# Performance work log

Hardware: AMD Instinct MI355X
Metric: run time of the kernel (lower is better)

Reference implementation:

```python
import jax, jax.numpy as jnp
import numpy as np

# --- model dims (from init_kwargs: d_model=2048, num_heads=16, d_conv=4, expand_v=2) ---
D_MODEL = 2048
N_HEADS = 16
D_HEAD = D_MODEL // N_HEADS          # 128
EXPAND_V = 2
KEY_DIM = N_HEADS * D_HEAD           # 2048
VALUE_DIM = KEY_DIM * EXPAND_V       # 4096
HEAD_V = D_HEAD * EXPAND_V           # 256
D_CONV = 4
CONV_CH = 2 * KEY_DIM + VALUE_DIM    # 8192 (q,k,v channels)
TOTAL_PROJ = 2 * KEY_DIM + 2 * VALUE_DIM + 2 * N_HEADS  # 12320
SPLITS = np.cumsum([KEY_DIM, KEY_DIM, VALUE_DIM, VALUE_DIM, N_HEADS]).tolist()


def setup_inputs() -> dict:
    key = jax.random.key(0)
    k0, k1, k2, k3 = jax.random.split(key, 4)
    B, L = 2, 2048
    return {
        "hidden_states": jax.random.normal(k0, (B, L, D_MODEL), jnp.float32),
        "W_qkvgba": jax.random.normal(k1, (D_MODEL, TOTAL_PROJ), jnp.float32) * 0.02,
        "W_conv": jax.random.normal(k2, (CONV_CH, D_CONV), jnp.float32) * 0.1,
        "A_log": jax.random.normal(k3, (N_HEADS,), jnp.float32) * 0.1,
        "dt_bias": jnp.zeros((N_HEADS,), jnp.float32),
    }


def _l2norm(x, eps=1e-6):
    return x * jax.lax.rsqrt(jnp.sum(x * x, axis=-1, keepdims=True) + eps)


def reference(hidden_states, W_qkvgba, W_conv, A_log, dt_bias):
    B, L, _ = hidden_states.shape
    # fused qkv / gate / beta / A projection
    proj = hidden_states @ W_qkvgba                      # [B, L, 12320]
    q, k, v, gate, b, A = jnp.split(proj, SPLITS, axis=-1)

    # depthwise causal short conv over q,k,v channels, then SiLU
    qkv = jnp.concatenate([q, k, v], axis=-1)            # [B, L, CONV_CH]
    x = qkv.transpose(0, 2, 1)                           # [B, C, L]
    kern = W_conv[:, None, :]                            # [C, 1, D_CONV]
    y = jax.lax.conv_general_dilated(
        x, kern, window_strides=(1,), padding=[(D_CONV - 1, 0)],
        feature_group_count=CONV_CH)
    y = jax.nn.silu(y).transpose(0, 2, 1)                # [B, L, C]
    q, k, v = jnp.split(y, [KEY_DIM, 2 * KEY_DIM], axis=-1)

    q = q.reshape(B, L, N_HEADS, D_HEAD)
    k = k.reshape(B, L, N_HEADS, D_HEAD)
    v = v.reshape(B, L, N_HEADS, HEAD_V)

    # L2 norm of q,k (use_qk_l2norm_in_kernel=True)
    q = _l2norm(q)
    k = _l2norm(k)
    scale = D_HEAD ** -0.5

    beta = jax.nn.sigmoid(b)                             # [B, L, H]
    g = -jnp.exp(A_log) * jax.nn.softplus(A + dt_bias)   # [B, L, H] (log decay <= 0)

    # gated delta-rule recurrence over time (scan); state S: [B, H, dk, dv]
    qT = q.transpose(1, 0, 2, 3)
    kT = k.transpose(1, 0, 2, 3)
    vT = v.transpose(1, 0, 2, 3)
    gT = g.transpose(1, 0, 2)
    bT = beta.transpose(1, 0, 2)

    def step(S, inp):
        qt, kt, vt, gt, bt = inp
        S = S * jnp.exp(gt)[..., None, None]
        kv = jnp.einsum('bhk,bhkv->bhv', kt, S)          # current memory readout at k
        delta = (vt - kv) * bt[..., None]                # delta-rule error, gated by beta
        S = S + jnp.einsum('bhk,bhv->bhkv', kt, delta)
        ot = jnp.einsum('bhk,bhkv->bhv', qt * scale, S)
        return S, ot

    S0 = jnp.zeros((B, N_HEADS, D_HEAD, HEAD_V), jnp.float32)
    _, oT = jax.lax.scan(step, S0, (qT, kT, vT, gT, bT))
    o = oT.transpose(1, 0, 2, 3)                         # [B, L, H, HEAD_V]

    # output gating: o * silu(gate)
    gate = gate.reshape(B, L, N_HEADS, HEAD_V)
    return o * jax.nn.silu(gate)
```

## Files before the change

### kernel.cpp

```cpp
#include <hip/hip_runtime.h>
#include <hip/hip_bf16.h>
#include <hip/hip_fp16.h>
#include <math.h>

#define L_SEQ 2048
#define DM    2048
#define NH    16
#define DH    128
#define HVD   256
#define NPROJ 12320
#define QKVW  8192
#define GW    4128

#define NTILE_N 97
#define KSTEPS  64

typedef _Float16 v8h __attribute__((ext_vector_type(8)));
typedef float f32x4 __attribute__((ext_vector_type(4)));

__device__ __forceinline__ void gload_lds16(const void* g, void* l) {
  __builtin_amdgcn_global_load_lds((const __attribute__((address_space(1))) void*)g,
                                   (__attribute__((address_space(3))) void*)l, 16, 0, 0);
}

__device__ __forceinline__ void splitw(float x, unsigned short& h, unsigned short& l) {
  _Float16 hh = (_Float16)x;
  _Float16 ll = (_Float16)(x - (float)hh);
  h = *(unsigned short*)&hh;
  l = *(unsigned short*)&ll;
}
__device__ __forceinline__ float h2f(unsigned short u) {
  return (float)(*(_Float16*)&u);
}

#define MFMA3(acc, ah, al, bh_, bl_)                                          \
  acc = __builtin_amdgcn_mfma_f32_16x16x32_f16(ah, bh_, acc, 0, 0, 0);        \
  acc = __builtin_amdgcn_mfma_f32_16x16x32_f16(ah, bl_, acc, 0, 0, 0);        \
  acc = __builtin_amdgcn_mfma_f32_16x16x32_f16(al, bh_, acc, 0, 0, 0);

__global__ __launch_bounds__(256) void pack_A_k(const float* __restrict__ H, _Float16* __restrict__ Ap) {
  const int mtile = blockIdx.x >> 6, kstep = blockIdx.x & 63;
  const size_t base = (size_t)blockIdx.x * 2 * 4096;
#pragma unroll
  for (int it = 0; it < 2; ++it) {
    int s = threadIdx.x + it * 256;
    int g = s >> 7, r = s & 127;
    const float* src = H + ((size_t)(mtile * 128 + r)) * 2048 + kstep * 32 + g * 8;
    float4 x0 = *(const float4*)src;
    float4 x1 = *(const float4*)(src + 4);
    float xs[8] = {x0.x, x0.y, x0.z, x0.w, x1.x, x1.y, x1.z, x1.w};
    v8h hi, lo;
#pragma unroll
    for (int j = 0; j < 8; ++j) {
      float v = xs[j] * 16.f;
      _Float16 h = (_Float16)v;
      hi[j] = h;
      lo[j] = (_Float16)(v - (float)h);
    }
    *(v8h*)(Ap + base + g * 1024 + r * 8) = hi;
    *(v8h*)(Ap + base + 4096 + g * 1024 + r * 8) = lo;
  }
}

__global__ __launch_bounds__(256) void pack_B_k(const float* __restrict__ W, _Float16* __restrict__ Bp) {
  const int ntile = blockIdx.x >> 6, kstep = blockIdx.x & 63;
  const size_t base = (size_t)blockIdx.x * 2 * 4096;
#pragma unroll
  for (int it = 0; it < 2; ++it) {
    int s = threadIdx.x + it * 256;
    int g = s >> 7, col = s & 127;
    int n = ntile * 128 + col;
    v8h hi, lo;
#pragma unroll
    for (int j = 0; j < 8; ++j) {
      int k = kstep * 32 + g * 8 + j;
      float v = (n < NPROJ) ? W[(size_t)k * NPROJ + n] * 1024.f : 0.f;
      _Float16 h = (_Float16)v;
      hi[j] = h;
      lo[j] = (_Float16)(v - (float)h);
    }
    *(v8h*)(Bp + base + g * 1024 + col * 8) = hi;
    *(v8h*)(Bp + base + 4096 + g * 1024 + col * 8) = lo;
  }
}

__global__ __launch_bounds__(512, 2) void gemm256_k(const _Float16* __restrict__ Ap,
                                                    const _Float16* __restrict__ Bp,
                                                    float* __restrict__ Cq,
                                                    float* __restrict__ Cg) {
  __shared__ _Float16 lds[2][32768];
  const int tid = threadIdx.x;
  const int supM = blockIdx.x & 15;
  const int supN = blockIdx.x >> 4;
  const int w = tid >> 6, lane = tid & 63;
  const int wm = w >> 2, wn = w & 3;
  const int lr = lane & 15, g16 = lane >> 4;

  f32x4 acc[8][4];
#pragma unroll
  for (int i = 0; i < 8; ++i)
#pragma unroll
    for (int j = 0; j < 4; ++j) acc[i][j] = (f32x4){0.f, 0.f, 0.f, 0.f};

  const size_t Ab0 = (size_t)(2 * supM) * KSTEPS * 8192;
  const size_t Ab1 = Ab0 + (size_t)KSTEPS * 8192;
  const size_t Bb0 = (size_t)(2 * supN) * KSTEPS * 8192;
  const size_t Bb1 = Bb0 + (size_t)KSTEPS * 8192;
  const int so = tid * 8;

#define STG(KS, BUF)                                                           \
  {                                                                            \
    const size_t ko = (size_t)(KS) * 8192;                                     \
    gload_lds16(Ap + Ab0 + ko + so,        &lds[BUF][so]);                     \
    gload_lds16(Ap + Ab0 + ko + so + 4096, &lds[BUF][so + 4096]);              \
    gload_lds16(Ap + Ab1 + ko + so,        &lds[BUF][8192 + so]);              \
    gload_lds16(Ap + Ab1 + ko + so + 4096, &lds[BUF][8192 + so + 4096]);       \
    gload_lds16(Bp + Bb0 + ko + so,        &lds[BUF][16384 + so]);             \
    gload_lds16(Bp + Bb0 + ko + so + 4096, &lds[BUF][16384 + so + 4096]);      \
    gload_lds16(Bp + Bb1 + ko + so,        &lds[BUF][24576 + so]);             \
    gload_lds16(Bp + Bb1 + ko + so + 4096, &lds[BUF][24576 + so + 4096]);      \
  }

  STG(0, 0);
  asm volatile("s_waitcnt vmcnt(0)" ::: "memory");
  __builtin_amdgcn_sched_barrier(0);
  __builtin_amdgcn_s_barrier();
  __builtin_amdgcn_sched_barrier(0);

  const int aoffB = wm * 8192 + lr * 8 + g16 * 1024;
  const int boffB = 16384 + (wn >> 1) * 8192 + ((wn & 1) * 64 + lr) * 8 + g16 * 1024;

  for (int kstep = 0; kstep < KSTEPS; ++kstep) {
    const int p = kstep & 1;
    if (kstep + 1 < KSTEPS) STG(kstep + 1, p ^ 1);

    v8h ah[8], al[8];
#pragma unroll
    for (int mb = 0; mb < 8; ++mb) {
      ah[mb] = *(const v8h*)&lds[p][aoffB + mb * 128];
      al[mb] = *(const v8h*)&lds[p][aoffB + mb * 128 + 4096];
    }
#pragma unroll
    for (int nt = 0; nt < 4; ++nt) {
      v8h bh = *(const v8h*)&lds[p][boffB + nt * 128];
      v8h bl = *(const v8h*)&lds[p][boffB + nt * 128 + 4096];
#pragma unroll
      for (int mb = 0; mb < 8; ++mb) {
        MFMA3(acc[mb][nt], ah[mb], al[mb], bh, bl);
      }
    }
    asm volatile("s_waitcnt vmcnt(0)" ::: "memory");
    __builtin_amdgcn_sched_barrier(0);
    __builtin_amdgcn_s_barrier();
    __builtin_amdgcn_sched_barrier(0);
  }
#undef STG

  const float sc = 1.f / 16384.f;
#pragma unroll
  for (int mb = 0; mb < 8; ++mb) {
#pragma unroll
    for (int nt = 0; nt < 4; ++nt) {
      int col = supN * 256 + wn * 64 + nt * 16 + lr;
#pragma unroll
      for (int r = 0; r < 4; ++r) {
        int row = supM * 256 + wm * 128 + mb * 16 + g16 * 4 + r;
        float v = acc[mb][nt][r] * sc;
        if (col < QKVW) Cq[(size_t)row * QKVW + col] = v;
        else            Cg[(size_t)row * GW + (col - QKVW)] = v;
      }
    }
  }
}

__global__ __launch_bounds__(256) void gemm_mfma_k(const _Float16* __restrict__ Ap,
                                                   const _Float16* __restrict__ Bp,
                                                   float* __restrict__ Cq,
                                                   float* __restrict__ Cg,
                                                   int ntile_base) {
  __shared__ _Float16 lds[2][16384];
  const int tid = threadIdx.x;
  const int mtile = blockIdx.x & 31;
  const int ntile = ntile_base + (blockIdx.x >> 5);
  const int wid = tid >> 6, lane = tid & 63;
  const int wm = wid >> 1, wn = wid & 1;
  const int lrow = lane & 15, g = lane >> 4;

  f32x4 acc[4][4];
#pragma unroll
  for (int i = 0; i < 4; ++i)
#pragma unroll
    for (int j = 0; j < 4; ++j) acc[i][j] = (f32x4){0.f, 0.f, 0.f, 0.f};

  const int aoff = (wm * 64 + lrow) * 8 + g * 1024;
  const int boff = (wn * 64 + lrow) * 8 + g * 1024;

  const _Float16* Asrc = Ap + ((size_t)(mtile * KSTEPS) * 2) * 4096 + tid * 8;
  const _Float16* Bsrc = Bp + ((size_t)(ntile * KSTEPS) * 2) * 4096 + tid * 8;

#define STAGE(KS, BUF)                                                         \
  {                                                                            \
    const _Float16* An_ = Asrc + (size_t)(KS) * 8192;                          \
    const _Float16* Bn_ = Bsrc + (size_t)(KS) * 8192;                          \
    _Pragma("unroll")                                                          \
    for (int r = 0; r < 4; ++r) {                                              \
      gload_lds16(An_ + r * 2048, &lds[BUF][r * 2048 + tid * 8]);              \
      gload_lds16(Bn_ + r * 2048, &lds[BUF][8192 + r * 2048 + tid * 8]);       \
    }                                                                          \
  }

  STAGE(0, 0);
  STAGE(1, 1);

  for (int kstep = 0; kstep < KSTEPS; ++kstep) {
    const int p = kstep & 1;
    if (kstep + 1 < KSTEPS) {
      asm volatile("s_waitcnt vmcnt(8)" ::: "memory");
    } else {
      asm volatile("s_waitcnt vmcnt(0)" ::: "memory");
    }
    __builtin_amdgcn_sched_barrier(0);
    __builtin_amdgcn_s_barrier();
    __builtin_amdgcn_sched_barrier(0);

    v8h ah[4], al[4], bh[4], bl[4];
#pragma unroll
    for (int f = 0; f < 4; ++f) {
      ah[f] = *(const v8h*)&lds[p][aoff + f * 128];
      al[f] = *(const v8h*)&lds[p][4096 + aoff + f * 128];
      bh[f] = *(const v8h*)&lds[p][8192 + boff + f * 128];
      bl[f] = *(const v8h*)&lds[p][12288 + boff + f * 128];
    }
#pragma unroll
    for (int fm = 0; fm < 4; ++fm)
#pragma unroll
      for (int fn = 0; fn < 4; ++fn) {
        acc[fm][fn] = __builtin_amdgcn_mfma_f32_16x16x32_f16(ah[fm], bh[fn], acc[fm][fn], 0, 0, 0);
        acc[fm][fn] = __builtin_amdgcn_mfma_f32_16x16x32_f16(ah[fm], bl[fn], acc[fm][fn], 0, 0, 0);
        acc[fm][fn] = __builtin_amdgcn_mfma_f32_16x16x32_f16(al[fm], bh[fn], acc[fm][fn], 0, 0, 0);
      }
    __builtin_amdgcn_sched_barrier(0);
    __builtin_amdgcn_s_barrier();
    __builtin_amdgcn_sched_barrier(0);
    if (kstep + 2 < KSTEPS) STAGE(kstep + 2, p);
  }
#undef STAGE

  const float sc = 1.f / 16384.f;
#pragma unroll
  for (int fm = 0; fm < 4; ++fm) {
    int row = mtile * 128 + wm * 64 + fm * 16 + g * 4;
#pragma unroll
    for (int fn = 0; fn < 4; ++fn) {
      int col = ntile * 128 + wn * 64 + fn * 16 + lrow;
      if (col < QKVW) {
#pragma unroll
        for (int r = 0; r < 4; ++r)
          Cq[(size_t)(row + r) * QKVW + col] = acc[fm][fn][r] * sc;
      } else if (col < NPROJ) {
        int lcol = col - QKVW;
#pragma unroll
        for (int r = 0; r < 4; ++r)
          Cg[(size_t)(row + r) * GW + lcol] = acc[fm][fn][r] * sc;
      }
    }
  }
}

__global__ __launch_bounds__(64) void conv_qk_k(
    const float* __restrict__ projQKV, const float* __restrict__ Wc,
    _Float16* __restrict__ qh, _Float16* __restrict__ ql,
    _Float16* __restrict__ kh, _Float16* __restrict__ kl)
{
  const int b = blockIdx.z, hg = blockIdx.y, tc = blockIdx.x;
  const int lane = threadIdx.x;
  const int ch = hg * 128 + lane * 2;
  float4 Wa = *(const float4*)(Wc + (size_t)ch * 4);
  float4 Wb = *(const float4*)(Wc + (size_t)ch * 4 + 4);
  const int t0 = tc * 64;
  const float* P = projQKV + (size_t)b * L_SEQ * QKVW + ch;
  float2 w0 = make_float2(0.f, 0.f), w1 = w0, w2 = w0;
  if (t0 >= 3) w0 = *(const float2*)(P + (size_t)(t0 - 3) * QKVW);
  if (t0 >= 2) w1 = *(const float2*)(P + (size_t)(t0 - 2) * QKVW);
  if (t0 >= 1) w2 = *(const float2*)(P + (size_t)(t0 - 1) * QKVW);
  const bool isq = hg < 16;
  const int h = isq ? hg : hg - 16;
  _Float16* dh = (isq ? qh : kh) + (((size_t)b * NH + h) * L_SEQ) * 128;
  _Float16* dl = (isq ? ql : kl) + (((size_t)b * NH + h) * L_SEQ) * 128;
  const float sc = (isq ? 0.08838834764831845f : 1.f) * 1024.f;
  for (int t = t0; t < t0 + 64; ++t) {
    float2 x = *(const float2*)(P + (size_t)t * QKVW);
    float y0 = w0.x * Wa.x + w1.x * Wa.y + w2.x * Wa.z + x.x * Wa.w;
    float y1 = w0.y * Wb.x + w1.y * Wb.y + w2.y * Wb.z + x.y * Wb.w;
    w0 = w1; w1 = w2; w2 = x;
    y0 = y0 / (1.f + expf(-y0));
    y1 = y1 / (1.f + expf(-y1));
    float ss = y0 * y0 + y1 * y1;
#pragma unroll
    for (int off = 1; off < 64; off <<= 1) ss += __shfl_xor(ss, off);
    float nrm = sc / sqrtf(ss + 1e-6f);
    unsigned short h0, l0, h1, l1;
    splitw(y0 * nrm, h0, l0);
    splitw(y1 * nrm, h1, l1);
    int idx = t * 128 + ((lane * 2) ^ ((t & 7) << 3));
    *(unsigned int*)&dh[idx] = (unsigned int)h0 | ((unsigned int)h1 << 16);
    *(unsigned int*)&dl[idx] = (unsigned int)l0 | ((unsigned int)l1 << 16);
  }
}

__global__ __launch_bounds__(256) void conv_v_k(
    const float* __restrict__ projQKV, const float* __restrict__ Wc,
    float* __restrict__ vn)
{
  const int b = blockIdx.z, cg = blockIdx.y, tc = blockIdx.x;
  const int vc = (cg * 256 + threadIdx.x) * 4;
  const int ch = 4096 + vc;
  float4 Wv0 = *(const float4*)(Wc + (size_t)ch * 4);
  float4 Wv1 = *(const float4*)(Wc + (size_t)ch * 4 + 4);
  float4 Wv2 = *(const float4*)(Wc + (size_t)ch * 4 + 8);
  float4 Wv3 = *(const float4*)(Wc + (size_t)ch * 4 + 12);
  const int t0 = tc * 64;
  const float* P = projQKV + (size_t)b * L_SEQ * QKVW + ch;
  float4 w0 = make_float4(0.f, 0.f, 0.f, 0.f), w1 = w0, w2 = w0;
  if (t0 >= 3) w0 = *(const float4*)(P + (size_t)(t0 - 3) * QKVW);
  if (t0 >= 2) w1 = *(const float4*)(P + (size_t)(t0 - 2) * QKVW);
  if (t0 >= 1) w2 = *(const float4*)(P + (size_t)(t0 - 1) * QKVW);
  const int h = vc >> 8, vcol = vc & 255;
  float* dst = vn + (((size_t)b * NH + h) * L_SEQ) * HVD + vcol;
  for (int t = t0; t < t0 + 64; ++t) {
    float4 x = *(const float4*)(P + (size_t)t * QKVW);
    float4 y;
    y.x = w0.x * Wv0.x + w1.x * Wv0.y + w2.x * Wv0.z + x.x * Wv0.w;
    y.y = w0.y * Wv1.x + w1.y * Wv1.y + w2.y * Wv1.z + x.y * Wv1.w;
    y.z = w0.z * Wv2.x + w1.z * Wv2.y + w2.z * Wv2.z + x.z * Wv2.w;
    y.w = w0.w * Wv3.x + w1.w * Wv3.y + w2.w * Wv3.z + x.w * Wv3.w;
    w0 = w1; w1 = w2; w2 = x;
    y.x = y.x / (1.f + expf(-y.x));
    y.y = y.y / (1.f + expf(-y.y));
    y.z = y.z / (1.f + expf(-y.z));
    y.w = y.w / (1.f + expf(-y.w));
    *(float4*)(dst + (size_t)t * HVD) = y;
  }
}

__global__ __launch_bounds__(256) void beta_g_k(
    const float* __restrict__ projGate, const float* __restrict__ A_log,
    const float* __restrict__ dt_bias, float* __restrict__ beta, float* __restrict__ g_out)
{
  int idx = blockIdx.x * 256 + threadIdx.x;
  if (idx >= 2 * NH * L_SEQ) return;
  int t = idx & (L_SEQ - 1);
  int h = (idx >> 11) & (NH - 1);
  int b = idx >> 15;
  size_t row = (size_t)(b * L_SEQ + t) * GW;
  float bv = projGate[row + 4096 + h];
  float av = projGate[row + 4112 + h];
  float be = 1.f / (1.f + expf(-bv));
  float xx = av + dt_bias[h];
  float sp = (xx > 20.f) ? xx : log1pf(expf(xx));
  float g = -expf(A_log[h]) * sp;
  beta[idx] = be;
  g_out[idx] = g;
}

__global__ __launch_bounds__(256) void p1_k(
    const _Float16* __restrict__ kh_g, const _Float16* __restrict__ kl_g,
    const _Float16* __restrict__ qh_g, const _Float16* __restrict__ ql_g,
    const float* __restrict__ g_arr, const float* __restrict__ beta_arr,
    _Float16* __restrict__ Tg_h, _Float16* __restrict__ Tg_l,
    _Float16* __restrict__ Hg_h, _Float16* __restrict__ Hg_l,
    _Float16* __restrict__ KTg_h, _Float16* __restrict__ KTg_l,
    float* __restrict__ coefG)
{
  __shared__ _Float16 Kh[8192], Kl[8192];
  __shared__ _Float16 QS[16384];
  __shared__ float lc[64], be[64], kw[64];
  _Float16* Qh = QS;
  _Float16* Ql = QS + 8192;
  float* Am = (float*)QS;
  float* Tm = Am + 4096;
  const int cid = blockIdx.x, bh = cid >> 5, ch = cid & 31, t0 = ch * 64;
  const int tid = threadIdx.x, w = tid >> 6, lane = tid & 63, lr = lane & 15, g16 = lane >> 4;

  const size_t gb = ((size_t)bh * 2048 + t0) * 128;
#pragma unroll
  for (int l = 0; l < 4; ++l) {
    int i = (tid + l * 256) * 8;
    gload_lds16(kh_g + gb + i, &Kh[i]);
    gload_lds16(kl_g + gb + i, &Kl[i]);
    gload_lds16(qh_g + gb + i, &Qh[i]);
    gload_lds16(ql_g + gb + i, &Ql[i]);
  }
  if (tid < 64) {
    float x = g_arr[(size_t)bh * 2048 + t0 + tid];
#pragma unroll
    for (int off = 1; off < 64; off <<= 1) { float y = __shfl_up(x, off); if (tid >= off) x += y; }
    lc[tid] = x;
    float x63 = __shfl(x, 63);
    float b_ = beta_arr[(size_t)bh * 2048 + t0 + tid];
    be[tid] = b_;
    kw[tid] = expf(x63 - x);
    float ca = expf(x);
    coefG[(size_t)cid * 192 + tid] = ca;
    coefG[(size_t)cid * 192 + 64 + tid] = b_;
    coefG[(size_t)cid * 192 + 128 + tid] = b_ * ca;
  }
  __syncthreads();
  const float ds20 = 1.f / 1048576.f;
  const int arow = w * 16 + lr, swa = (arow & 7) << 3;
  f32x4 gacc[4];
  for (int nt = 0; nt < 4; ++nt) {
    f32x4 acc = (f32x4){0.f, 0.f, 0.f, 0.f};
    int nrow = nt * 16 + lr, swn = (nrow & 7) << 3;
#pragma unroll
    for (int ks = 0; ks < 4; ++ks) {
      int c = ks * 32 + g16 * 8;
      v8h ah = *(const v8h*)&Kh[arow * 128 + (c ^ swa)];
      v8h al = *(const v8h*)&Kl[arow * 128 + (c ^ swa)];
      v8h bhh = *(const v8h*)&Kh[nrow * 128 + (c ^ swn)];
      v8h bll = *(const v8h*)&Kl[nrow * 128 + (c ^ swn)];
      MFMA3(acc, ah, al, bhh, bll);
    }
    gacc[nt] = acc;
  }
  for (int nt = 0; nt < 4; ++nt) {
    f32x4 acc = (f32x4){0.f, 0.f, 0.f, 0.f};
    int nrow = nt * 16 + lr, swn = (nrow & 7) << 3;
#pragma unroll
    for (int ks = 0; ks < 4; ++ks) {
      int c = ks * 32 + g16 * 8;
      v8h ah = *(const v8h*)&Qh[arow * 128 + (c ^ swa)];
      v8h al = *(const v8h*)&Ql[arow * 128 + (c ^ swa)];
      v8h bhh = *(const v8h*)&Kh[nrow * 128 + (c ^ swn)];
      v8h bll = *(const v8h*)&Kl[nrow * 128 + (c ^ swn)];
      MFMA3(acc, ah, al, bhh, bll);
    }
    int s_ = nt * 16 + lr;
#pragma unroll
    for (int r = 0; r < 4; ++r) {
      int t = w * 16 + g16 * 4 + r;
      float hv = (s_ <= t) ? acc[r] * ds20 * expf(lc[t] - lc[s_]) : 0.f;
      unsigned short hh, ll; splitw(hv * 16384.f, hh, ll);
      size_t go = (size_t)cid * 4096 + t * 64 + (s_ ^ ((t & 7) << 3));
      *(unsigned short*)&Hg_h[go] = hh;
      *(unsigned short*)&Hg_l[go] = ll;
    }
  }
  __syncthreads();
  for (int nt = 0; nt < 4; ++nt) {
    int s_ = nt * 16 + lr;
#pragma unroll
    for (int r = 0; r < 4; ++r) {
      int t = w * 16 + g16 * 4 + r;
      float av = (s_ < t) ? gacc[nt][r] * ds20 * be[t] * expf(lc[t] - lc[s_]) : 0.f;
      Am[t * 64 + s_] = av;
    }
  }
#pragma unroll
  for (int l = 0; l < 16; ++l) { int s2 = tid + l * 256; Tm[s2] = ((s2 >> 6) == (s2 & 63)) ? 1.f : 0.f; }
  for (int s = tid; s < 8192; s += 256) {
    int feat = s >> 6, t = s & 63;
    int ki = t * 128 + (feat ^ ((t & 7) << 3));
    float kvv = ((float)Kh[ki] + (float)Kl[ki]) * kw[t];
    unsigned short hh, ll; splitw(kvv, hh, ll);
    size_t go = (size_t)cid * 8192 + feat * 64 + (t ^ ((feat & 7) << 3));
    *(unsigned short*)&KTg_h[go] = hh;
    *(unsigned short*)&KTg_l[go] = ll;
  }
  __syncthreads();
  if (w == 0) {
    int j = lane;
    for (int t = 1; t < 64; ++t) {
      float sum = 0.f;
      for (int s = 0; s < t; ++s) sum = fmaf(Am[t * 64 + s], Tm[s * 64 + j], sum);
      Tm[t * 64 + j] = ((j == t) ? 1.f : 0.f) - sum;
    }
  }
  __syncthreads();
#pragma unroll
  for (int l = 0; l < 16; ++l) {
    int s2 = tid + l * 256;
    int t = s2 >> 6, sc_ = s2 & 63;
    unsigned short hh, ll; splitw(Tm[s2] * 256.f, hh, ll);
    size_t go = (size_t)cid * 4096 + t * 64 + (sc_ ^ ((t & 7) << 3));
    *(unsigned short*)&Tg_h[go] = hh;
    *(unsigned short*)&Tg_l[go] = ll;
  }
}

__global__ __launch_bounds__(256) void p2_k(
    const _Float16* __restrict__ qh_g, const _Float16* __restrict__ ql_g,
    const _Float16* __restrict__ kh_g, const _Float16* __restrict__ kl_g,
    const float* __restrict__ vn, const float* __restrict__ projGate,
    const _Float16* __restrict__ Tg_h, const _Float16* __restrict__ Tg_l,
    const _Float16* __restrict__ Hg_h, const _Float16* __restrict__ Hg_l,
    const _Float16* __restrict__ KTg_h, const _Float16* __restrict__ KTg_l,
    const float* __restrict__ coefG, float* __restrict__ out)
{
  __shared__ _Float16 St_h[4096], St_l[4096];
  __shared__ _Float16 KQ0[8192], KQ1[8192];
  __shared__ _Float16 KK0[8192], KK1[8192];
  __shared__ _Float16 KTs_h[8192], KTs_l[8192];
  __shared__ _Float16 Ts_h[4096], Ts_l[4096];
  __shared__ _Float16 Hs_h[4096], Hs_l[4096];
  __shared__ float cf[192];

  const int blk = blockIdx.x;
  const int vb = blk >> 5, bh = blk & 31;
  const int b = bh >> 4, h = bh & 15, v0 = vb * 32;
  const int tid = threadIdx.x, w = tid >> 6, lane = tid & 63, lr = lane & 15, g16 = lane >> 4;

  _Float16* BT_h = &KQ0[0];
  _Float16* BT_l = &KQ0[4096];
  _Float16* UT_h = &KQ1[0];
  _Float16* UT_l = &KQ1[4096];

#pragma unroll
  for (int l = 0; l < 8; ++l) { ((unsigned int*)St_h)[tid + l * 256] = 0u; }
#pragma unroll
  for (int l = 0; l < 8; ++l) { ((unsigned int*)St_l)[tid + l * 256] = 0u; }

  const float* gp = projGate + ((size_t)b * 2048) * GW + h * 256 + v0;
  const float i2_16 = 1.f / 65536.f;
  const float i2_20 = 1.f / 1048576.f;
  const float uscale = 1.f / 256.f;
  const float sscale = 64.f / 65536.f;

  for (int ch = 0; ch < 32; ++ch) {
    const int cid = bh * 32 + ch, t0 = ch * 64;
    {
      const _Float16* th = Tg_h + (size_t)cid * 4096;
      const _Float16* tl = Tg_l + (size_t)cid * 4096;
      const _Float16* hh = Hg_h + (size_t)cid * 4096;
      const _Float16* hl = Hg_l + (size_t)cid * 4096;
      const _Float16* kth = KTg_h + (size_t)cid * 8192;
      const _Float16* ktl = KTg_l + (size_t)cid * 8192;
      const size_t gb = ((size_t)bh * 2048 + t0) * 128;
#pragma unroll
      for (int l = 0; l < 2; ++l) {
        int i = (tid + l * 256) * 8;
        gload_lds16(th + i, &Ts_h[i]);
        gload_lds16(tl + i, &Ts_l[i]);
        gload_lds16(hh + i, &Hs_h[i]);
        gload_lds16(hl + i, &Hs_l[i]);
      }
#pragma unroll
      for (int l = 0; l < 4; ++l) {
        int i = (tid + l * 256) * 8;
        gload_lds16(kth + i, &KTs_h[i]);
        gload_lds16(ktl + i, &KTs_l[i]);
        gload_lds16(qh_g + gb + i, &KQ0[i]);
        gload_lds16(ql_g + gb + i, &KQ1[i]);
        gload_lds16(kh_g + gb + i, &KK0[i]);
        gload_lds16(kl_g + gb + i, &KK1[i]);
      }
      if (tid < 48) gload_lds16(coefG + (size_t)cid * 192 + tid * 4, &cf[tid * 4]);
    }
    float Vv[2][4];
#pragma unroll
    for (int nt = 0; nt < 2; ++nt)
#pragma unroll
      for (int r = 0; r < 4; ++r)
        Vv[nt][r] = vn[((size_t)bh * 2048 + t0 + w * 16 + g16 * 4 + r) * 256 + v0 + nt * 16 + lr];
    __syncthreads();
    const float cc = cf[63];
    const int arow = w * 16 + lr, swa = (arow & 7) << 3;
    f32x4 Oacc[2];
    {
      for (int nt = 0; nt < 2; ++nt) {
        f32x4 acc = (f32x4){0.f, 0.f, 0.f, 0.f};
        const int n = nt * 16 + lr, swn = (n & 7) << 3;
#pragma unroll
        for (int ks = 0; ks < 4; ++ks) {
          int c = ks * 32 + g16 * 8;
          v8h ah = *(const v8h*)&KQ0[arow * 128 + (c ^ swa)];
          v8h al = *(const v8h*)&KQ1[arow * 128 + (c ^ swa)];
          v8h bhh = *(const v8h*)&St_h[n * 128 + (c ^ swn)];
          v8h bll = *(const v8h*)&St_l[n * 128 + (c ^ swn)];
          MFMA3(acc, ah, al, bhh, bll);
        }
        Oacc[nt] = acc;
      }
      float4 cav = *(float4*)&cf[w * 16 + g16 * 4];
#pragma unroll
      for (int nt = 0; nt < 2; ++nt) {
        Oacc[nt][0] *= cav.x * 16.f; Oacc[nt][1] *= cav.y * 16.f;
        Oacc[nt][2] *= cav.z * 16.f; Oacc[nt][3] *= cav.w * 16.f;
      }
    }
    ushort4 pBh[2], pBl[2];
    {
      float4 cb1v = *(float4*)&cf[64 + w * 16 + g16 * 4];
      float4 cb2v = *(float4*)&cf[128 + w * 16 + g16 * 4];
      for (int nt = 0; nt < 2; ++nt) {
        f32x4 acc = (f32x4){0.f, 0.f, 0.f, 0.f};
        const int n = nt * 16 + lr, swn = (n & 7) << 3;
#pragma unroll
        for (int ks = 0; ks < 4; ++ks) {
          int c = ks * 32 + g16 * 8;
          v8h ah = *(const v8h*)&KK0[arow * 128 + (c ^ swa)];
          v8h al = *(const v8h*)&KK1[arow * 128 + (c ^ swa)];
          v8h bhh = *(const v8h*)&St_h[n * 128 + (c ^ swn)];
          v8h bll = *(const v8h*)&St_l[n * 128 + (c ^ swn)];
          MFMA3(acc, ah, al, bhh, bll);
        }
        float cb1a[4] = {cb1v.x, cb1v.y, cb1v.z, cb1v.w};
        float cb2a[4] = {cb2v.x, cb2v.y, cb2v.z, cb2v.w};
        unsigned short* ph = (unsigned short*)&pBh[nt];
        unsigned short* pl = (unsigned short*)&pBl[nt];
#pragma unroll
        for (int r = 0; r < 4; ++r) {
          float kv = acc[r] * i2_16;
          float Bv = cb1a[r] * Vv[nt][r] - cb2a[r] * kv;
          splitw(Bv * 64.f, ph[r], pl[r]);
        }
      }
    }
    __syncthreads();
    {
      const int tb = w * 16 + g16 * 4;
      for (int nt = 0; nt < 2; ++nt) {
        const int n = nt * 16 + lr, swn = (n & 7) << 3;
        int ad = n * 64 + (tb ^ swn);
        *(ushort4*)&BT_h[ad] = pBh[nt];
        *(ushort4*)&BT_l[ad] = pBl[nt];
      }
    }
    __syncthreads();
    {
      const int tb = w * 16 + g16 * 4;
      for (int nt = 0; nt < 2; ++nt) {
        f32x4 acc = (f32x4){0.f, 0.f, 0.f, 0.f};
        const int n = nt * 16 + lr, swn = (n & 7) << 3;
#pragma unroll
        for (int ks = 0; ks < 2; ++ks) {
          int c = ks * 32 + g16 * 8;
          v8h ah = *(const v8h*)&Ts_h[arow * 64 + (c ^ swa)];
          v8h al = *(const v8h*)&Ts_l[arow * 64 + (c ^ swa)];
          v8h bhh = *(const v8h*)&BT_h[n * 64 + (c ^ swn)];
          v8h bll = *(const v8h*)&BT_l[n * 64 + (c ^ swn)];
          MFMA3(acc, ah, al, bhh, bll);
        }
        ushort4 H, L;
        unsigned short* ph = (unsigned short*)&H;
        unsigned short* pl = (unsigned short*)&L;
#pragma unroll
        for (int r = 0; r < 4; ++r) splitw(acc[r] * uscale, ph[r], pl[r]);
        int ad = n * 64 + (tb ^ swn);
        *(ushort4*)&UT_h[ad] = H;
        *(ushort4*)&UT_l[ad] = L;
      }
    }
    __syncthreads();
    {
      for (int nt = 0; nt < 2; ++nt) {
        const int n = nt * 16 + lr, swn = (n & 7) << 3;
#pragma unroll
        for (int ks = 0; ks < 2; ++ks) {
          int c = ks * 32 + g16 * 8;
          v8h ah = *(const v8h*)&Hs_h[arow * 64 + (c ^ swa)];
          v8h al = *(const v8h*)&Hs_l[arow * 64 + (c ^ swa)];
          v8h bhh = *(const v8h*)&UT_h[n * 64 + (c ^ swn)];
          v8h bll = *(const v8h*)&UT_l[n * 64 + (c ^ swn)];
          MFMA3(Oacc[nt], ah, al, bhh, bll);
        }
      }
      for (int nt = 0; nt < 2; ++nt) {
        const int n = nt * 16 + lr;
#pragma unroll
        for (int r = 0; r < 4; ++r) {
          int t = t0 + w * 16 + g16 * 4 + r;
          float Ov = Oacc[nt][r] * i2_20;
          float gv = gp[(size_t)t * GW + n];
          out[((size_t)b * 2048 + t) * 4096 + h * 256 + v0 + n] = Ov * (gv / (1.f + expf(-gv)));
        }
      }
      const float cc1024 = cc * 1024.f;
#pragma unroll
      for (int m2 = w * 2; m2 < w * 2 + 2; ++m2) {
        const int ar2 = m2 * 16 + lr, swa2 = (ar2 & 7) << 3;
        const int fb = m2 * 16 + g16 * 4;
        for (int nt = 0; nt < 2; ++nt) {
          const int n = nt * 16 + lr, swn = (n & 7) << 3;
          int sad = n * 128 + (fb ^ swn);
          ushort4 sh4 = *(ushort4*)&St_h[sad];
          ushort4 sl4 = *(ushort4*)&St_l[sad];
          f32x4 acc;
          acc[0] = cc1024 * (h2f(sh4.x) + h2f(sl4.x));
          acc[1] = cc1024 * (h2f(sh4.y) + h2f(sl4.y));
          acc[2] = cc1024 * (h2f(sh4.z) + h2f(sl4.z));
          acc[3] = cc1024 * (h2f(sh4.w) + h2f(sl4.w));
#pragma unroll
          for (int ks = 0; ks < 2; ++ks) {
            int c = ks * 32 + g16 * 8;
            v8h ah = *(const v8h*)&KTs_h[ar2 * 64 + (c ^ swa2)];
            v8h al = *(const v8h*)&KTs_l[ar2 * 64 + (c ^ swa2)];
            v8h bhh = *(const v8h*)&UT_h[n * 64 + (c ^ swn)];
            v8h bll = *(const v8h*)&UT_l[n * 64 + (c ^ swn)];
            MFMA3(acc, ah, al, bhh, bll);
          }
          ushort4 H, L;
          unsigned short* ph = (unsigned short*)&H;
          unsigned short* pl = (unsigned short*)&L;
#pragma unroll
          for (int r = 0; r < 4; ++r) splitw(acc[r] * sscale, ph[r], pl[r]);
          *(ushort4*)&St_h[sad] = H;
          *(ushort4*)&St_l[sad] = L;
        }
      }
    }
    __syncthreads();
  }
}

extern "C" void kernel_launch(void* const* d_in, const int* in_sizes, int n_in,
                              void* d_out, int out_size, void* d_ws, size_t ws_size,
                              hipStream_t stream) {
  const float* hidden  = (const float*)d_in[0];
  const float* W       = (const float*)d_in[1];
  const float* Wc      = (const float*)d_in[2];
  const float* A_log   = (const float*)d_in[3];
  const float* dt_bias = (const float*)d_in[4];
  float* out = (float*)d_out;

  char* ws = (char*)d_ws;
  _Float16* Ap = (_Float16*)ws;
  _Float16* Bp = (_Float16*)(ws + (size_t)33554432);
  _Float16* qh = (_Float16*)ws;
  _Float16* ql = (_Float16*)(ws + (size_t)16777216);
  _Float16* kh = (_Float16*)(ws + (size_t)33554432);
  _Float16* kl = (_Float16*)(ws + (size_t)50331648);
  float* vn    = (float*)(ws + (size_t)67108864);
  float* g_arr = (float*)(ws + (size_t)134217728);
  float* beta  = (float*)(ws + (size_t)134479872);
  float* projQKV = (float*)(ws + (size_t)135266304);
  char*  tb0 = ws + (size_t)135266304;
  _Float16* Tg_h  = (_Float16*)tb0;
  _Float16* Tg_l  = (_Float16*)(tb0 + (size_t)8388608);
  _Float16* Hg_h  = (_Float16*)(tb0 + (size_t)16777216);
  _Float16* Hg_l  = (_Float16*)(tb0 + (size_t)25165824);
  _Float16* KTg_h = (_Float16*)(tb0 + (size_t)33554432);
  _Float16* KTg_l = (_Float16*)(tb0 + (size_t)50331648);
  float*    coefG = (float*)   (tb0 + (size_t)67108864);
  float* projGate = (float*)(ws + (size_t)269484032);

  pack_A_k<<<32 * KSTEPS, 256, 0, stream>>>(hidden, Ap);
  pack_B_k<<<NTILE_N * KSTEPS, 256, 0, stream>>>(W, Bp);
  gemm256_k<<<16 * 48, 512, 0, stream>>>(Ap, Bp, projQKV, projGate);
  gemm_mfma_k<<<32, 256, 0, stream>>>(Ap, Bp, projQKV, projGate, 96);

  conv_qk_k<<<dim3(32, 32, 2), 64, 0, stream>>>(projQKV, Wc, qh, ql, kh, kl);
  conv_v_k<<<dim3(32, 4, 2), 256, 0, stream>>>(projQKV, Wc, vn);
  beta_g_k<<<(2 * NH * L_SEQ + 255) / 256, 256, 0, stream>>>(projGate, A_log, dt_bias, beta, g_arr);

  p1_k<<<1024, 256, 0, stream>>>(kh, kl, qh, ql, g_arr, beta, Tg_h, Tg_l, Hg_h, Hg_l, KTg_h, KTg_l, coefG);
  p2_k<<<256, 256, 0, stream>>>(qh, ql, kh, kl, vn, projGate, Tg_h, Tg_l, Hg_h, Hg_l, KTg_h, KTg_l, coefG, out);
}
```

Before: 971.4 us.

## Split-K the narrow gate/beta tail GEMM and reduce partials in beta_g

The leftover 32 projection columns (the beta and A logits) were handled by 32 blocks, each computing a full 128x128 tile over all K steps, so most of the work and time went to padding and a long serial K loop. They are now computed by 128 blocks that split K four ways and produce only the 32 valid columns. Each block writes partial sums to a scratch buffer that aliases the already-consumed packed-B region, and beta_g_k sums the four partials. The risks are the aliasing of workspace and the extra partial-buffer traffic.

Measured after the change: 927.9 us (median of 2 runs). 4.5% less time.

```diff
diff --git a/kernel.cpp b/kernel.cpp
--- a/kernel.cpp
+++ b/kernel.cpp
@@ -173,98 +173,60 @@
   }
 }
 
-__global__ __launch_bounds__(256) void gemm_mfma_k(const _Float16* __restrict__ Ap,
-                                                   const _Float16* __restrict__ Bp,
-                                                   float* __restrict__ Cq,
-                                                   float* __restrict__ Cg,
-                                                   int ntile_base) {
-  __shared__ _Float16 lds[2][16384];
+__global__ __launch_bounds__(256) void tail_k(const _Float16* __restrict__ Ap,
+                                              const _Float16* __restrict__ Bp,
+                                              float* __restrict__ partial) {
+  __shared__ _Float16 lds[16384];
+  const int bid = blockIdx.x;
+  const int kseg = bid >> 5, mtile = bid & 31;
   const int tid = threadIdx.x;
-  const int mtile = blockIdx.x & 31;
-  const int ntile = ntile_base + (blockIdx.x >> 5);
-  const int wid = tid >> 6, lane = tid & 63;
-  const int wm = wid >> 1, wn = wid & 1;
-  const int lrow = lane & 15, g = lane >> 4;
-
-  f32x4 acc[4][4];
-#pragma unroll
-  for (int i = 0; i < 4; ++i)
-#pragma unroll
-    for (int j = 0; j < 4; ++j) acc[i][j] = (f32x4){0.f, 0.f, 0.f, 0.f};
-
-  const int aoff = (wm * 64 + lrow) * 8 + g * 1024;
-  const int boff = (wn * 64 + lrow) * 8 + g * 1024;
+  const int wid = tid >> 6, lane = tid & 63, lr = lane & 15, g16 = lane >> 4;
+
+  f32x4 acc[2][2];
+#pragma unroll
+  for (int i = 0; i < 2; ++i)
+#pragma unroll
+    for (int j = 0; j < 2; ++j) acc[i][j] = (f32x4){0.f, 0.f, 0.f, 0.f};
 
   const _Float16* Asrc = Ap + ((size_t)(mtile * KSTEPS) * 2) * 4096 + tid * 8;
-  const _Float16* Bsrc = Bp + ((size_t)(ntile * KSTEPS) * 2) * 4096 + tid * 8;
-
-#define STAGE(KS, BUF)                                                         \
-  {                                                                            \
-    const _Float16* An_ = Asrc + (size_t)(KS) * 8192;                          \
-    const _Float16* Bn_ = Bsrc + (size_t)(KS) * 8192;                          \
-    _Pragma("unroll")                                                          \
-    for (int r = 0; r < 4; ++r) {                                              \
-      gload_lds16(An_ + r * 2048, &lds[BUF][r * 2048 + tid * 8]);              \
-      gload_lds16(Bn_ + r * 2048, &lds[BUF][8192 + r * 2048 + tid * 8]);       \
-    }                                                                          \
-  }
-
-  STAGE(0, 0);
-  STAGE(1, 1);
-
-  for (int kstep = 0; kstep < KSTEPS; ++kstep) {
-    const int p = kstep & 1;
-    if (kstep + 1 < KSTEPS) {
-      asm volatile("s_waitcnt vmcnt(8)" ::: "memory");
-    } else {
-      asm volatile("s_waitcnt vmcnt(0)" ::: "memory");
-    }
-    __builtin_amdgcn_sched_barrier(0);
-    __builtin_amdgcn_s_barrier();
-    __builtin_amdgcn_sched_barrier(0);
-
-    v8h ah[4], al[4], bh[4], bl[4];
-#pragma unroll
-    for (int f = 0; f < 4; ++f) {
-      ah[f] = *(const v8h*)&lds[p][aoff + f * 128];
-      al[f] = *(const v8h*)&lds[p][4096 + aoff + f * 128];
-      bh[f] = *(const v8h*)&lds[p][8192 + boff + f * 128];
-      bl[f] = *(const v8h*)&lds[p][12288 + boff + f * 128];
-    }
-#pragma unroll
-    for (int fm = 0; fm < 4; ++fm)
-#pragma unroll
-      for (int fn = 0; fn < 4; ++fn) {
-        acc[fm][fn] = __builtin_amdgcn_mfma_f32_16x16x32_f16(ah[fm], bh[fn], acc[fm][fn], 0, 0, 0);
-        acc[fm][fn] = __builtin_amdgcn_mfma_f32_16x16x32_f16(ah[fm], bl[fn], acc[fm][fn], 0, 0, 0);
-        acc[fm][fn] = __builtin_amdgcn_mfma_f32_16x16x32_f16(al[fm], bh[fn], acc[fm][fn], 0, 0, 0);
-      }
-    __builtin_amdgcn_sched_barrier(0);
-    __builtin_amdgcn_s_barrier();
-    __builtin_amdgcn_sched_barrier(0);
-    if (kstep + 2 < KSTEPS) STAGE(kstep + 2, p);
-  }
-#undef STAGE
+  const _Float16* Bsrc = Bp + ((size_t)(96 * KSTEPS) * 2) * 4096 + tid * 8;
+
+  for (int ks = kseg * 16; ks < kseg * 16 + 16; ++ks) {
+    __syncthreads();
+#pragma unroll
+    for (int r = 0; r < 4; ++r) {
+      gload_lds16(Asrc + (size_t)ks * 8192 + r * 2048, &lds[r * 2048 + tid * 8]);
+      gload_lds16(Bsrc + (size_t)ks * 8192 + r * 2048, &lds[8192 + r * 2048 + tid * 8]);
+    }
+    __syncthreads();
+    const int abase = g16 * 1024;
+#pragma unroll
+    for (int fm = 0; fm < 2; ++fm) {
+      int row = wid * 32 + fm * 16 + lr;
+      v8h ah = *(const v8h*)&lds[abase + row * 8];
+      v8h al = *(const v8h*)&lds[4096 + abase + row * 8];
+#pragma unroll
+      for (int fn = 0; fn < 2; ++fn) {
+        int col = fn * 16 + lr;
+        v8h bh = *(const v8h*)&lds[8192 + abase + col * 8];
+        v8h bl = *(const v8h*)&lds[12288 + abase + col * 8];
+        MFMA3(acc[fm][fn], ah, al, bh, bl);
+      }
+    }
+  }
 
   const float sc = 1.f / 16384.f;
 #pragma unroll
-  for (int fm = 0; fm < 4; ++fm) {
-    int row = mtile * 128 + wm * 64 + fm * 16 + g * 4;
-#pragma unroll
-    for (int fn = 0; fn < 4; ++fn) {
-      int col = ntile * 128 + wn * 64 + fn * 16 + lrow;
-      if (col < QKVW) {
-#pragma unroll
-        for (int r = 0; r < 4; ++r)
-          Cq[(size_t)(row + r) * QKVW + col] = acc[fm][fn][r] * sc;
-      } else if (col < NPROJ) {
-        int lcol = col - QKVW;
-#pragma unroll
-        for (int r = 0; r < 4; ++r)
-          Cg[(size_t)(row + r) * GW + lcol] = acc[fm][fn][r] * sc;
-      }
-    }
-  }
+  for (int fm = 0; fm < 2; ++fm)
+#pragma unroll
+    for (int fn = 0; fn < 2; ++fn) {
+      int col = fn * 16 + lr;
+#pragma unroll
+      for (int r = 0; r < 4; ++r) {
+        int row = mtile * 128 + wid * 32 + fm * 16 + g16 * 4 + r;
+        partial[((size_t)kseg * 4096 + row) * 32 + col] = acc[fm][fn][r] * sc;
+      }
+    }
 }
 
 __global__ __launch_bounds__(64) void conv_qk_k(
@@ -344,7 +306,7 @@
 }
 
 __global__ __launch_bounds__(256) void beta_g_k(
-    const float* __restrict__ projGate, const float* __restrict__ A_log,
+    const float* __restrict__ partial, const float* __restrict__ A_log,
     const float* __restrict__ dt_bias, float* __restrict__ beta, float* __restrict__ g_out)
 {
   int idx = blockIdx.x * 256 + threadIdx.x;
@@ -352,9 +314,13 @@
   int t = idx & (L_SEQ - 1);
   int h = (idx >> 11) & (NH - 1);
   int b = idx >> 15;
-  size_t row = (size_t)(b * L_SEQ + t) * GW;
-  float bv = projGate[row + 4096 + h];
-  float av = projGate[row + 4112 + h];
+  size_t row = (size_t)(b * L_SEQ + t);
+  float bv = 0.f, av = 0.f;
+#pragma unroll
+  for (int s = 0; s < 4; ++s) {
+    bv += partial[((size_t)s * 4096 + row) * 32 + h];
+    av += partial[((size_t)s * 4096 + row) * 32 + 16 + h];
+  }
   float be = 1.f / (1.f + expf(-bv));
   float xx = av + dt_bias[h];
   float sp = (xx > 20.f) ? xx : log1pf(expf(xx));
@@ -726,6 +692,7 @@
   char* ws = (char*)d_ws;
   _Float16* Ap = (_Float16*)ws;
   _Float16* Bp = (_Float16*)(ws + (size_t)33554432);
+  float* partial = (float*)(ws + (size_t)33554432);
   _Float16* qh = (_Float16*)ws;
   _Float16* ql = (_Float16*)(ws + (size_t)16777216);
   _Float16* kh = (_Float16*)(ws + (size_t)33554432);
@@ -746,12 +713,12 @@
 
   pack_A_k<<<32 * KSTEPS, 256, 0, stream>>>(hidden, Ap);
   pack_B_k<<<NTILE_N * KSTEPS, 256, 0, stream>>>(W, Bp);
-  gemm256_k<<<16 * 48, 512, 0, stream>>>(Ap, Bp, projQKV, projGate);
-  gemm_mfma_k<<<32, 256, 0, stream>>>(Ap, Bp, projQKV, projGate, 96);
+  gemm256_k<<<768, 512, 0, stream>>>(Ap, Bp, projQKV, projGate);
+  tail_k<<<128, 256, 0, stream>>>(Ap, Bp, partial);
+  beta_g_k<<<(2 * NH * L_SEQ + 255) / 256, 256, 0, stream>>>(partial, A_log, dt_bias, beta, g_arr);
 
   conv_qk_k<<<dim3(32, 32, 2), 64, 0, stream>>>(projQKV, Wc, qh, ql, kh, kl);
   conv_v_k<<<dim3(32, 4, 2), 256, 0, stream>>>(projQKV, Wc, vn);
-  beta_g_k<<<(2 * NH * L_SEQ + 255) / 256, 256, 0, stream>>>(projGate, A_log, dt_bias, beta, g_arr);
 
   p1_k<<<1024, 256, 0, stream>>>(kh, kl, qh, ql, g_arr, beta, Tg_h, Tg_l, Hg_h, Hg_l, KTg_h, KTg_l, coefG);
   p2_k<<<256, 256, 0, stream>>>(qh, ql, kh, kl, vn, projGate, Tg_h, Tg_l, Hg_h, Hg_l, KTg_h, KTg_l, coefG, out);
```
